# Performance work log

Hardware: AMD Instinct MI355X
Metric: run time of the kernel (lower is better)

## Reference

```python
import jax, jax.numpy as jnp
import numpy as np

N_NODES = 46080   # 512 graphs x 90 nodes
NPG = 90          # nodes per graph (AAL atlas)
G = 512           # number of graphs
E = 737280        # edges (degree 16)
IN_DIM = 90
H = 64            # hidden_channels
K = 70            # sort-pool k


def setup_inputs() -> dict:
    key = jax.random.key(0)
    ks = jax.random.split(key, 12)
    x = jax.random.normal(ks[0], (N_NODES, IN_DIM), dtype=jnp.float32)
    # intra-graph random edges: src/dst within each graph's 90-node block
    gidx = jnp.repeat(jnp.arange(G, dtype=jnp.int64), E // G) * NPG
    src = jax.random.randint(ks[1], (E,), 0, NPG, dtype=jnp.int64) + gidx
    dst = jax.random.randint(ks[2], (E,), 0, NPG, dtype=jnp.int64) + gidx
    edge_index = jnp.stack([src, dst])
    edge_weight = jax.random.uniform(ks[3], (E,), dtype=jnp.float32)
    batch = jnp.repeat(jnp.arange(G, dtype=jnp.int64), NPG)
    s1 = 1.0 / np.sqrt(IN_DIM)
    s2 = 1.0 / np.sqrt(H)
    sk = 1.0 / np.sqrt(H * K)
    W1 = jax.random.uniform(ks[4], (IN_DIM, H), jnp.float32, -s1, s1)
    b1 = jnp.zeros((H,), jnp.float32)
    W2 = jax.random.uniform(ks[5], (H, H), jnp.float32, -s2, s2)
    b2 = jnp.zeros((H,), jnp.float32)
    lw1 = jax.random.uniform(ks[6], (H * K, H), jnp.float32, -sk, sk)
    lb1 = jax.random.uniform(ks[7], (H,), jnp.float32, -sk, sk)
    lw2 = jax.random.uniform(ks[8], (H, 1), jnp.float32, -s2, s2)
    lb2 = jax.random.uniform(ks[9], (1,), jnp.float32, -s2, s2)
    return {"x": x, "edge_index": edge_index, "edge_weight": edge_weight,
            "batch": batch, "W1": W1, "b1": b1, "W2": W2, "b2": b2,
            "lw1": lw1, "lb1": lb1, "lw2": lw2, "lb2": lb2}


def _gcn_conv(x, W, b, src, dst, ew, n):
    # PyG GCNConv: add self-loops (weight 1), symmetric normalization,
    # message = norm * (x @ W)[src], scatter-add to dst, add bias.
    xw = x @ W
    loop = jnp.arange(n)
    src_f = jnp.concatenate([src, loop])
    dst_f = jnp.concatenate([dst, loop])
    ew_f = jnp.concatenate([ew, jnp.ones((n,), x.dtype)])
    deg = jax.ops.segment_sum(ew_f, dst_f, num_segments=n)
    dinv = jnp.where(deg > 0, jax.lax.rsqrt(jnp.maximum(deg, 1e-12)), 0.0)
    norm = dinv[src_f] * ew_f * dinv[dst_f]
    msg = xw[src_f] * norm[:, None]          # [E+n, H] irregular gather
    out = jax.ops.segment_sum(msg, dst_f, num_segments=n)
    return out + b


def reference(x, edge_index, edge_weight, batch, W1, b1, W2, b2, lw1, lb1, lw2, lb2):
    src, dst = edge_index[0], edge_index[1]
    h1 = _gcn_conv(x, W1, b1, src, dst, edge_weight, N_NODES)
    x_train = h1
    h = jax.nn.relu(h1)
    h2 = _gcn_conv(h, W2, b2, src, dst, edge_weight, N_NODES)
    # global_sort_pool: per graph, sort nodes descending by last channel, keep top K.
    # batch is contiguous with NPG nodes/graph, so a reshape is exact.
    hg = h2.reshape(G, NPG, H)
    order = jnp.argsort(-hg[:, :, -1], axis=1)          # [G, NPG] descending
    hs = jnp.take_along_axis(hg, order[:, :, None], axis=1)
    pooled = hs[:, :K, :].reshape(G, K * H)
    # F.dropout(p=0.5, training=False) -> identity at inference
    z = pooled @ lw1 + lb1
    z = z @ lw2 + lb2
    out = jax.nn.sigmoid(z).squeeze(-1)                  # [G]
    return out, x_train
```

## Files before the change

### kernel.cpp

```cpp
#include <hip/hip_runtime.h>


#define NG      512
#define NPG     90
#define EPG     1440
#define IN_DIM  90
#define HD      64
#define KP      70
#define E_TOT   (NG*EPG)
#define NT      512

__global__ __launch_bounds__(256) void weff_fold(
    const float* __restrict__ lw1, const float* __restrict__ lb1,
    const float* __restrict__ lw2, const float* __restrict__ lb2,
    float* __restrict__ ws)
{
    int i = blockIdx.x*256 + threadIdx.x;
    if (i < KP*HD) {
        const float4* row = (const float4*)(lw1 + (size_t)i*HD);
        const float4* w   = (const float4*)lw2;
        float s = 0.f;
        #pragma unroll
        for (int j4 = 0; j4 < HD/4; ++j4) {
            float4 r = row[j4], v = w[j4];
            s += r.x*v.x + r.y*v.y + r.z*v.z + r.w*v.w;
        }
        ws[i] = s;
    } else if (i == KP*HD) {
        float s = lb2[0];
        for (int j = 0; j < HD; ++j) s += lb1[j]*lw2[j];
        ws[KP*HD] = s;
    }
}

__global__ __launch_bounds__(NT, 4) void dgcnn_fused(
    const float* __restrict__ x,
    const int*   __restrict__ ei,
    const float* __restrict__ ew,
    const float* __restrict__ W1,
    const float* __restrict__ b1,
    const float* __restrict__ W2,
    const float* __restrict__ b2,
    const float* __restrict__ weff,
    float* __restrict__ out,
    float* __restrict__ xtrain)
{
    __shared__ float sB[NPG*HD];
    __shared__ float sC[NPG*HD];
    __shared__ float s_dinv[NPG];
    __shared__ int   s_indeg[NPG];
    __shared__ int   s_cursor[NPG];
    __shared__ int   s_rowstart[NPG+1];
    __shared__ unsigned s_epack[EPG];
    __shared__ int   s_ranknode[KP];
    __shared__ float s_red[8];

    const int g = blockIdx.x;
    const int t = threadIdx.x;
    const int j = t & 63;
    const int grp = t >> 6;
    const int ebase = g*EPG;
    const int nbase = g*NPG;

    if (t < NPG) { s_dinv[t] = 1.0f; s_indeg[t] = 0; }
    __syncthreads();

    for (int e = t; e < EPG; e += NT) {
        int d = ei[E_TOT + ebase + e] - nbase;
        float w = ew[ebase + e];
        atomicAdd(&s_dinv[d], w);
        atomicAdd(&s_indeg[d], 1);
    }
    for (int i4 = t; i4 < IN_DIM*HD/4; i4 += NT)
        ((float4*)sC)[i4] = ((const float4*)W1)[i4];
    __syncthreads();

    if (t < NPG) s_dinv[t] = rsqrtf(fmaxf(s_dinv[t], 1e-12f));
    if (t <= NPG) {
        int acc = 0;
        for (int i = 0; i < t; ++i) acc += s_indeg[i];
        s_rowstart[t] = acc;
        if (t < NPG) s_cursor[t] = acc;
    }
    __syncthreads();

    for (int e = t; e < EPG; e += NT) {
        int s = ei[ebase + e] - nbase;
        int d = ei[E_TOT + ebase + e] - nbase;
        float nrm = s_dinv[s] * ew[ebase + e] * s_dinv[d];
        int pos = atomicAdd(&s_cursor[d], 1);
        s_epack[pos] = (__float_as_uint(nrm) & ~127u) | (unsigned)s;
    }
    __syncthreads();

    const float* xg = x + (size_t)nbase * IN_DIM;
    for (int it = 0; it < 3; ++it) {
        int r0 = it*32 + grp*4;
        int rr0 = min(r0+0, NPG-1), rr1 = min(r0+1, NPG-1);
        int rr2 = min(r0+2, NPG-1), rr3 = min(r0+3, NPG-1);
        const float2* xp0 = (const float2*)(xg + rr0*IN_DIM);
        const float2* xp1 = (const float2*)(xg + rr1*IN_DIM);
        const float2* xp2 = (const float2*)(xg + rr2*IN_DIM);
        const float2* xp3 = (const float2*)(xg + rr3*IN_DIM);
        float a0 = 0.f, a1 = 0.f, a2 = 0.f, a3 = 0.f;
        #pragma unroll 9
        for (int kh = 0; kh < IN_DIM/2; ++kh) {
            float w0 = sC[(2*kh)*HD + j];
            float w1 = sC[(2*kh+1)*HD + j];
            float2 v0 = xp0[kh], v1 = xp1[kh], v2 = xp2[kh], v3 = xp3[kh];
            a0 += v0.x*w0 + v0.y*w1;
            a1 += v1.x*w0 + v1.y*w1;
            a2 += v2.x*w0 + v2.y*w1;
            a3 += v3.x*w0 + v3.y*w1;
        }
        if (r0+0 < NPG) sB[(r0+0)*HD + j] = a0;
        if (r0+1 < NPG) sB[(r0+1)*HD + j] = a1;
        if (r0+2 < NPG) sB[(r0+2)*HD + j] = a2;
        if (r0+3 < NPG) sB[(r0+3)*HD + j] = a3;
    }
    __syncthreads();

    float* xt = xtrain + (size_t)nbase * HD;
    for (int o = t; o < NPG*HD; o += NT) {
        int d = o >> 6, c = o & 63;
        float dv = s_dinv[d];
        float a = dv*dv*sB[o];
        int p0 = s_rowstart[d], p1 = s_rowstart[d+1];
        for (int p = p0; p < p1; ++p) {
            unsigned u = s_epack[p];
            a += __uint_as_float(u & ~127u) * sB[(int)(u & 127u)*HD + c];
        }
        a += b1[c];
        xt[o] = a;
        sC[o] = fmaxf(a, 0.f);
    }
    __syncthreads();

    for (int it = 0; it < 3; ++it) {
        int r0 = it*32 + grp*4;
        int rr0 = min(r0+0, NPG-1), rr1 = min(r0+1, NPG-1);
        int rr2 = min(r0+2, NPG-1), rr3 = min(r0+3, NPG-1);
        float a0 = 0.f, a1 = 0.f, a2 = 0.f, a3 = 0.f;
        #pragma unroll 4
        for (int k4 = 0; k4 < HD/4; ++k4) {
            int k = k4*4;
            float4 h0 = *(const float4*)&sC[rr0*HD + k];
            float4 h1 = *(const float4*)&sC[rr1*HD + k];
            float4 h2 = *(const float4*)&sC[rr2*HD + k];
            float4 h3 = *(const float4*)&sC[rr3*HD + k];
            float w0 = W2[(k+0)*HD + j];
            float w1 = W2[(k+1)*HD + j];
            float w2 = W2[(k+2)*HD + j];
            float w3 = W2[(k+3)*HD + j];
            a0 += h0.x*w0 + h0.y*w1 + h0.z*w2 + h0.w*w3;
            a1 += h1.x*w0 + h1.y*w1 + h1.z*w2 + h1.w*w3;
            a2 += h2.x*w0 + h2.y*w1 + h2.z*w2 + h2.w*w3;
            a3 += h3.x*w0 + h3.y*w1 + h3.z*w2 + h3.w*w3;
        }
        if (r0+0 < NPG) sB[(r0+0)*HD + j] = a0;
        if (r0+1 < NPG) sB[(r0+1)*HD + j] = a1;
        if (r0+2 < NPG) sB[(r0+2)*HD + j] = a2;
        if (r0+3 < NPG) sB[(r0+3)*HD + j] = a3;
    }
    __syncthreads();

    for (int o = t; o < NPG*HD; o += NT) {
        int d = o >> 6, c = o & 63;
        float dv = s_dinv[d];
        float a = dv*dv*sB[o];
        int p0 = s_rowstart[d], p1 = s_rowstart[d+1];
        for (int p = p0; p < p1; ++p) {
            unsigned u = s_epack[p];
            a += __uint_as_float(u & ~127u) * sB[(int)(u & 127u)*HD + c];
        }
        sC[o] = a + b2[c];
    }
    __syncthreads();

    if (t < NPG) {
        float vi = sC[t*HD + (HD-1)];
        int rank = 0;
        for (int jj = 0; jj < NPG; ++jj) {
            float vj = sC[jj*HD + (HD-1)];
            rank += (vj > vi) || (vj == vi && jj < t);
        }
        if (rank < KP) s_ranknode[rank] = t;
    }
    __syncthreads();

    float part = 0.f;
    #pragma unroll
    for (int m = 0; m < 9; ++m) {
        int i = t + m*NT;
        if (i < KP*HD) {
            int k = i >> 6, c = i & 63;
            part += weff[i] * sC[s_ranknode[k]*HD + c];
        }
    }
    #pragma unroll
    for (int off = 32; off > 0; off >>= 1) part += __shfl_down(part, off, 64);
    if (j == 0) s_red[grp] = part;
    __syncthreads();
    if (t == 0) {
        float zz = weff[KP*HD];
        #pragma unroll
        for (int m = 0; m < 8; ++m) zz += s_red[m];
        out[g] = 1.0f / (1.0f + expf(-zz));
    }
}

extern "C" void kernel_launch(void* const* d_in, const int* in_sizes, int n_in,
                              void* d_out, int out_size, void* d_ws, size_t ws_size,
                              hipStream_t stream) {
    const float* x   = (const float*)d_in[0];
    const int*   ei  = (const int*)  d_in[1];
    const float* ew  = (const float*)d_in[2];
    const float* W1  = (const float*)d_in[4];
    const float* b1  = (const float*)d_in[5];
    const float* W2  = (const float*)d_in[6];
    const float* b2  = (const float*)d_in[7];
    const float* lw1 = (const float*)d_in[8];
    const float* lb1 = (const float*)d_in[9];
    const float* lw2 = (const float*)d_in[10];
    const float* lb2 = (const float*)d_in[11];

    float* ws     = (float*)d_ws;
    float* out    = (float*)d_out;
    float* xtrain = out + NG;

    weff_fold<<<(KP*HD + 256)/256, 256, 0, stream>>>(lw1, lb1, lw2, lb2, ws);
    dgcnn_fused<<<NG, NT, 0, stream>>>(x, ei, ew, W1, b1, W2, b2,
                                       ws, out, xtrain);
}
```

Before: 182.3 us.

## Double block size to 1024 threads and parallelize scan, rank and W2 staging

Raises threads per block from 512 to 1024 so each graph's dense transforms, aggregation and readout use more lanes. The serial per-thread prefix sum over in-degrees becomes a wave-level shuffle scan, and the O(N^2) rank computation for sort-pooling is split across 8 lanes per node with a shuffle reduction. W2 is staged into shared memory instead of being read from global memory inside the inner loop. The larger block and extra shared memory lower how many blocks fit per CU and add register pressure under the 1024-thread launch bound, which may reduce occupancy.

After: 254.8 us. 1.4x slower.

```diff
diff --git a/kernel.cpp b/kernel.cpp
--- a/kernel.cpp
+++ b/kernel.cpp
@@ -8,7 +8,7 @@
 #define HD      64
 #define KP      70
 #define E_TOT   (NG*EPG)
-#define NT      512
+#define NT      1024
 
 __global__ __launch_bounds__(256) void weff_fold(
     const float* __restrict__ lw1, const float* __restrict__ lb1,
@@ -33,7 +33,7 @@
     }
 }
 
-__global__ __launch_bounds__(NT, 4) void dgcnn_fused(
+__global__ __launch_bounds__(NT, 8) void dgcnn_fused(
     const float* __restrict__ x,
     const int*   __restrict__ ei,
     const float* __restrict__ ew,
@@ -47,13 +47,15 @@
 {
     __shared__ float sB[NPG*HD];
     __shared__ float sC[NPG*HD];
+    __shared__ float sW2[HD*HD];
     __shared__ float s_dinv[NPG];
     __shared__ int   s_indeg[NPG];
     __shared__ int   s_cursor[NPG];
     __shared__ int   s_rowstart[NPG+1];
     __shared__ unsigned s_epack[EPG];
     __shared__ int   s_ranknode[KP];
-    __shared__ float s_red[8];
+    __shared__ float s_red[16];
+    __shared__ int   s_itmp;
 
     const int g = blockIdx.x;
     const int t = threadIdx.x;
@@ -76,11 +78,22 @@
     __syncthreads();
 
     if (t < NPG) s_dinv[t] = rsqrtf(fmaxf(s_dinv[t], 1e-12f));
-    if (t <= NPG) {
-        int acc = 0;
-        for (int i = 0; i < t; ++i) acc += s_indeg[i];
-        s_rowstart[t] = acc;
-        if (t < NPG) s_cursor[t] = acc;
+    {
+        int vi = (t < NPG) ? s_indeg[t] : 0;
+        int inc = vi;
+        #pragma unroll
+        for (int d = 1; d < 64; d <<= 1) {
+            int up = __shfl_up(inc, d, 64);
+            if ((t & 63) >= d) inc += up;
+        }
+        if (t == 63) s_itmp = inc;
+        __syncthreads();
+        if (t <= NPG) {
+            int base = (grp == 1) ? s_itmp : 0;
+            int excl = inc - vi + base;
+            s_rowstart[t] = excl;
+            if (t < NPG) s_cursor[t] = excl;
+        }
     }
     __syncthreads();
 
@@ -94,29 +107,31 @@
     __syncthreads();
 
     const float* xg = x + (size_t)nbase * IN_DIM;
-    for (int it = 0; it < 3; ++it) {
-        int r0 = it*32 + grp*4;
-        int rr0 = min(r0+0, NPG-1), rr1 = min(r0+1, NPG-1);
-        int rr2 = min(r0+2, NPG-1), rr3 = min(r0+3, NPG-1);
-        const float2* xp0 = (const float2*)(xg + rr0*IN_DIM);
-        const float2* xp1 = (const float2*)(xg + rr1*IN_DIM);
-        const float2* xp2 = (const float2*)(xg + rr2*IN_DIM);
-        const float2* xp3 = (const float2*)(xg + rr3*IN_DIM);
-        float a0 = 0.f, a1 = 0.f, a2 = 0.f, a3 = 0.f;
-        #pragma unroll 9
-        for (int kh = 0; kh < IN_DIM/2; ++kh) {
-            float w0 = sC[(2*kh)*HD + j];
-            float w1 = sC[(2*kh+1)*HD + j];
-            float2 v0 = xp0[kh], v1 = xp1[kh], v2 = xp2[kh], v3 = xp3[kh];
-            a0 += v0.x*w0 + v0.y*w1;
-            a1 += v1.x*w0 + v1.y*w1;
-            a2 += v2.x*w0 + v2.y*w1;
-            a3 += v3.x*w0 + v3.y*w1;
-        }
-        if (r0+0 < NPG) sB[(r0+0)*HD + j] = a0;
-        if (r0+1 < NPG) sB[(r0+1)*HD + j] = a1;
-        if (r0+2 < NPG) sB[(r0+2)*HD + j] = a2;
-        if (r0+3 < NPG) sB[(r0+3)*HD + j] = a3;
+    for (int it = 0; it < 2; ++it) {
+        int r0 = it*64 + grp*4;
+        if (r0 < NPG) {
+            int rr0 = min(r0+0, NPG-1), rr1 = min(r0+1, NPG-1);
+            int rr2 = min(r0+2, NPG-1), rr3 = min(r0+3, NPG-1);
+            const float2* xp0 = (const float2*)(xg + rr0*IN_DIM);
+            const float2* xp1 = (const float2*)(xg + rr1*IN_DIM);
+            const float2* xp2 = (const float2*)(xg + rr2*IN_DIM);
+            const float2* xp3 = (const float2*)(xg + rr3*IN_DIM);
+            float a0 = 0.f, a1 = 0.f, a2 = 0.f, a3 = 0.f;
+            #pragma unroll 9
+            for (int kh = 0; kh < IN_DIM/2; ++kh) {
+                float w0 = sC[(2*kh)*HD + j];
+                float w1 = sC[(2*kh+1)*HD + j];
+                float2 v0 = xp0[kh], v1 = xp1[kh], v2 = xp2[kh], v3 = xp3[kh];
+                a0 += v0.x*w0 + v0.y*w1;
+                a1 += v1.x*w0 + v1.y*w1;
+                a2 += v2.x*w0 + v2.y*w1;
+                a3 += v3.x*w0 + v3.y*w1;
+            }
+            if (r0+0 < NPG) sB[(r0+0)*HD + j] = a0;
+            if (r0+1 < NPG) sB[(r0+1)*HD + j] = a1;
+            if (r0+2 < NPG) sB[(r0+2)*HD + j] = a2;
+            if (r0+3 < NPG) sB[(r0+3)*HD + j] = a3;
+        }
     }
     __syncthreads();
 
@@ -134,33 +149,37 @@
         xt[o] = a;
         sC[o] = fmaxf(a, 0.f);
     }
-    __syncthreads();
-
-    for (int it = 0; it < 3; ++it) {
-        int r0 = it*32 + grp*4;
-        int rr0 = min(r0+0, NPG-1), rr1 = min(r0+1, NPG-1);
-        int rr2 = min(r0+2, NPG-1), rr3 = min(r0+3, NPG-1);
-        float a0 = 0.f, a1 = 0.f, a2 = 0.f, a3 = 0.f;
-        #pragma unroll 4
-        for (int k4 = 0; k4 < HD/4; ++k4) {
-            int k = k4*4;
-            float4 h0 = *(const float4*)&sC[rr0*HD + k];
-            float4 h1 = *(const float4*)&sC[rr1*HD + k];
-            float4 h2 = *(const float4*)&sC[rr2*HD + k];
-            float4 h3 = *(const float4*)&sC[rr3*HD + k];
-            float w0 = W2[(k+0)*HD + j];
-            float w1 = W2[(k+1)*HD + j];
-            float w2 = W2[(k+2)*HD + j];
-            float w3 = W2[(k+3)*HD + j];
-            a0 += h0.x*w0 + h0.y*w1 + h0.z*w2 + h0.w*w3;
-            a1 += h1.x*w0 + h1.y*w1 + h1.z*w2 + h1.w*w3;
-            a2 += h2.x*w0 + h2.y*w1 + h2.z*w2 + h2.w*w3;
-            a3 += h3.x*w0 + h3.y*w1 + h3.z*w2 + h3.w*w3;
-        }
-        if (r0+0 < NPG) sB[(r0+0)*HD + j] = a0;
-        if (r0+1 < NPG) sB[(r0+1)*HD + j] = a1;
-        if (r0+2 < NPG) sB[(r0+2)*HD + j] = a2;
-        if (r0+3 < NPG) sB[(r0+3)*HD + j] = a3;
+    for (int i4 = t; i4 < HD*HD/4; i4 += NT)
+        ((float4*)sW2)[i4] = ((const float4*)W2)[i4];
+    __syncthreads();
+
+    for (int it = 0; it < 2; ++it) {
+        int r0 = it*64 + grp*4;
+        if (r0 < NPG) {
+            int rr0 = min(r0+0, NPG-1), rr1 = min(r0+1, NPG-1);
+            int rr2 = min(r0+2, NPG-1), rr3 = min(r0+3, NPG-1);
+            float a0 = 0.f, a1 = 0.f, a2 = 0.f, a3 = 0.f;
+            #pragma unroll 4
+            for (int k4 = 0; k4 < HD/4; ++k4) {
+                int k = k4*4;
+                float4 h0 = *(const float4*)&sC[rr0*HD + k];
+                float4 h1 = *(const float4*)&sC[rr1*HD + k];
+                float4 h2 = *(const float4*)&sC[rr2*HD + k];
+                float4 h3 = *(const float4*)&sC[rr3*HD + k];
+                float w0 = sW2[(k+0)*HD + j];
+                float w1 = sW2[(k+1)*HD + j];
+                float w2 = sW2[(k+2)*HD + j];
+                float w3 = sW2[(k+3)*HD + j];
+                a0 += h0.x*w0 + h0.y*w1 + h0.z*w2 + h0.w*w3;
+                a1 += h1.x*w0 + h1.y*w1 + h1.z*w2 + h1.w*w3;
+                a2 += h2.x*w0 + h2.y*w1 + h2.z*w2 + h2.w*w3;
+                a3 += h3.x*w0 + h3.y*w1 + h3.z*w2 + h3.w*w3;
+            }
+            if (r0+0 < NPG) sB[(r0+0)*HD + j] = a0;
+            if (r0+1 < NPG) sB[(r0+1)*HD + j] = a1;
+            if (r0+2 < NPG) sB[(r0+2)*HD + j] = a2;
+            if (r0+3 < NPG) sB[(r0+3)*HD + j] = a3;
+        }
     }
     __syncthreads();
 
@@ -177,20 +196,28 @@
     }
     __syncthreads();
 
-    if (t < NPG) {
-        float vi = sC[t*HD + (HD-1)];
-        int rank = 0;
-        for (int jj = 0; jj < NPG; ++jj) {
-            float vj = sC[jj*HD + (HD-1)];
-            rank += (vj > vi) || (vj == vi && jj < t);
-        }
-        if (rank < KP) s_ranknode[rank] = t;
+    if (t < NPG*8) {
+        int n = t >> 3, q = t & 7;
+        float vi = sC[n*HD + (HD-1)];
+        int cnt = 0;
+        #pragma unroll 12
+        for (int m = 0; m < 12; ++m) {
+            int jj = q*12 + m;
+            if (jj < NPG) {
+                float vj = sC[jj*HD + (HD-1)];
+                cnt += (vj > vi) || (vj == vi && jj < n);
+            }
+        }
+        cnt += __shfl_down(cnt, 4, 8);
+        cnt += __shfl_down(cnt, 2, 8);
+        cnt += __shfl_down(cnt, 1, 8);
+        if (q == 0 && cnt < KP) s_ranknode[cnt] = n;
     }
     __syncthreads();
 
     float part = 0.f;
     #pragma unroll
-    for (int m = 0; m < 9; ++m) {
+    for (int m = 0; m < 5; ++m) {
         int i = t + m*NT;
         if (i < KP*HD) {
             int k = i >> 6, c = i & 63;
@@ -204,7 +231,7 @@
     if (t == 0) {
         float zz = weff[KP*HD];
         #pragma unroll
-        for (int m = 0; m < 8; ++m) zz += s_red[m];
+        for (int m = 0; m < 16; ++m) zz += s_red[m];
         out[g] = 1.0f / (1.0f + expf(-zz));
     }
 }
```

## Split fused DGCNN kernel into CSR, GEMM, scatter and final-pool stages

Applied to the files above, without the earlier changes.

Breaks the single per-graph fused kernel into five launches: CSR and normalisation build (with the weight fold merged in), a row-tiled x@W1 GEMM, a first aggregation split four ways by column quarter, a row-tiled GEMM with ReLU, and a per-graph second aggregation with sort-pool and readout. The goal is far more, and lighter, blocks for the GEMMs and the first scatter than the 512 heavy-LDS blocks of the fused version. In exchange, intermediates (packed edges, row starts, xw, h@W2) make round trips through global memory and there are extra kernel launches.

Measured after the change: 177.5 us. 2.7% less time.

```diff
diff --git a/kernel.cpp b/kernel.cpp
--- a/kernel.cpp
+++ b/kernel.cpp
@@ -8,74 +8,36 @@
 #define HD      64
 #define KP      70
 #define E_TOT   (NG*EPG)
-#define NT      512
-
-__global__ __launch_bounds__(256) void weff_fold(
+
+#define WEFF_OFF   0
+#define EPACK_OFF  4608
+#define RS_OFF     (EPACK_OFF + NG*EPG)
+#define D2_OFF     (RS_OFF + NG*96)
+#define HW2_OFF    (D2_OFF + NG*96)
+
+__global__ __launch_bounds__(256) void k0_csr(
+    const int* __restrict__ ei, const float* __restrict__ ew,
     const float* __restrict__ lw1, const float* __restrict__ lb1,
     const float* __restrict__ lw2, const float* __restrict__ lb2,
     float* __restrict__ ws)
 {
-    int i = blockIdx.x*256 + threadIdx.x;
-    if (i < KP*HD) {
-        const float4* row = (const float4*)(lw1 + (size_t)i*HD);
-        const float4* w   = (const float4*)lw2;
-        float s = 0.f;
-        #pragma unroll
-        for (int j4 = 0; j4 < HD/4; ++j4) {
-            float4 r = row[j4], v = w[j4];
-            s += r.x*v.x + r.y*v.y + r.z*v.z + r.w*v.w;
-        }
-        ws[i] = s;
-    } else if (i == KP*HD) {
-        float s = lb2[0];
-        for (int j = 0; j < HD; ++j) s += lb1[j]*lw2[j];
-        ws[KP*HD] = s;
-    }
-}
-
-__global__ __launch_bounds__(NT, 4) void dgcnn_fused(
-    const float* __restrict__ x,
-    const int*   __restrict__ ei,
-    const float* __restrict__ ew,
-    const float* __restrict__ W1,
-    const float* __restrict__ b1,
-    const float* __restrict__ W2,
-    const float* __restrict__ b2,
-    const float* __restrict__ weff,
-    float* __restrict__ out,
-    float* __restrict__ xtrain)
-{
-    __shared__ float sB[NPG*HD];
-    __shared__ float sC[NPG*HD];
-    __shared__ float s_dinv[NPG];
+    __shared__ float s_deg[NPG];
     __shared__ int   s_indeg[NPG];
+    __shared__ int   s_rowstart[NPG+1];
     __shared__ int   s_cursor[NPG];
-    __shared__ int   s_rowstart[NPG+1];
-    __shared__ unsigned s_epack[EPG];
-    __shared__ int   s_ranknode[KP];
-    __shared__ float s_red[8];
-
-    const int g = blockIdx.x;
-    const int t = threadIdx.x;
-    const int j = t & 63;
-    const int grp = t >> 6;
-    const int ebase = g*EPG;
-    const int nbase = g*NPG;
-
-    if (t < NPG) { s_dinv[t] = 1.0f; s_indeg[t] = 0; }
-    __syncthreads();
-
-    for (int e = t; e < EPG; e += NT) {
+
+    const int g = blockIdx.x, t = threadIdx.x;
+    const int ebase = g*EPG, nbase = g*NPG;
+
+    if (t < NPG) { s_deg[t] = 1.0f; s_indeg[t] = 0; }
+    __syncthreads();
+    for (int e = t; e < EPG; e += 256) {
         int d = ei[E_TOT + ebase + e] - nbase;
-        float w = ew[ebase + e];
-        atomicAdd(&s_dinv[d], w);
+        atomicAdd(&s_deg[d], ew[ebase + e]);
         atomicAdd(&s_indeg[d], 1);
     }
-    for (int i4 = t; i4 < IN_DIM*HD/4; i4 += NT)
-        ((float4*)sC)[i4] = ((const float4*)W1)[i4];
-    __syncthreads();
-
-    if (t < NPG) s_dinv[t] = rsqrtf(fmaxf(s_dinv[t], 1e-12f));
+    __syncthreads();
+    if (t < NPG) s_deg[t] = rsqrtf(fmaxf(s_deg[t], 1e-12f));
     if (t <= NPG) {
         int acc = 0;
         for (int i = 0; i < t; ++i) acc += s_indeg[i];
@@ -84,93 +46,175 @@
     }
     __syncthreads();
 
-    for (int e = t; e < EPG; e += NT) {
+    unsigned* epk = (unsigned*)ws + EPACK_OFF + g*EPG;
+    for (int e = t; e < EPG; e += 256) {
         int s = ei[ebase + e] - nbase;
         int d = ei[E_TOT + ebase + e] - nbase;
-        float nrm = s_dinv[s] * ew[ebase + e] * s_dinv[d];
+        float nrm = s_deg[s] * ew[ebase + e] * s_deg[d];
         int pos = atomicAdd(&s_cursor[d], 1);
-        s_epack[pos] = (__float_as_uint(nrm) & ~127u) | (unsigned)s;
-    }
-    __syncthreads();
-
-    const float* xg = x + (size_t)nbase * IN_DIM;
-    for (int it = 0; it < 3; ++it) {
-        int r0 = it*32 + grp*4;
-        int rr0 = min(r0+0, NPG-1), rr1 = min(r0+1, NPG-1);
-        int rr2 = min(r0+2, NPG-1), rr3 = min(r0+3, NPG-1);
-        const float2* xp0 = (const float2*)(xg + rr0*IN_DIM);
-        const float2* xp1 = (const float2*)(xg + rr1*IN_DIM);
-        const float2* xp2 = (const float2*)(xg + rr2*IN_DIM);
-        const float2* xp3 = (const float2*)(xg + rr3*IN_DIM);
-        float a0 = 0.f, a1 = 0.f, a2 = 0.f, a3 = 0.f;
-        #pragma unroll 9
-        for (int kh = 0; kh < IN_DIM/2; ++kh) {
-            float w0 = sC[(2*kh)*HD + j];
-            float w1 = sC[(2*kh+1)*HD + j];
-            float2 v0 = xp0[kh], v1 = xp1[kh], v2 = xp2[kh], v3 = xp3[kh];
-            a0 += v0.x*w0 + v0.y*w1;
-            a1 += v1.x*w0 + v1.y*w1;
-            a2 += v2.x*w0 + v2.y*w1;
-            a3 += v3.x*w0 + v3.y*w1;
-        }
-        if (r0+0 < NPG) sB[(r0+0)*HD + j] = a0;
-        if (r0+1 < NPG) sB[(r0+1)*HD + j] = a1;
-        if (r0+2 < NPG) sB[(r0+2)*HD + j] = a2;
-        if (r0+3 < NPG) sB[(r0+3)*HD + j] = a3;
-    }
-    __syncthreads();
-
-    float* xt = xtrain + (size_t)nbase * HD;
-    for (int o = t; o < NPG*HD; o += NT) {
+        epk[pos] = (__float_as_uint(nrm) & ~127u) | (unsigned)s;
+    }
+    if (t <= NPG) ((int*)ws)[RS_OFF + g*96 + t] = s_rowstart[t];
+    if (t < NPG)  ws[D2_OFF + g*96 + t] = s_deg[t]*s_deg[t];
+
+    int i = g*256 + t;
+    if (g < 18) {
+        if (i < KP*HD) {
+            const float4* row = (const float4*)(lw1 + (size_t)i*HD);
+            const float4* w   = (const float4*)lw2;
+            float s = 0.f;
+            #pragma unroll
+            for (int j4 = 0; j4 < HD/4; ++j4) {
+                float4 r = row[j4], v = w[j4];
+                s += r.x*v.x + r.y*v.y + r.z*v.z + r.w*v.w;
+            }
+            ws[WEFF_OFF + i] = s;
+        } else if (i == KP*HD) {
+            float s = lb2[0];
+            for (int jj = 0; jj < HD; ++jj) s += lb1[jj]*lw2[jj];
+            ws[WEFF_OFF + KP*HD] = s;
+        }
+    }
+}
+
+__global__ __launch_bounds__(256) void k1_gemm1(
+    const float* __restrict__ x, const float* __restrict__ W1,
+    float* __restrict__ xw)
+{
+    __shared__ float sx[16*IN_DIM];
+    const int t = threadIdx.x;
+    const int row0 = blockIdx.x * 16;
+
+    const float4* gx = (const float4*)(x + (size_t)row0*IN_DIM);
+    for (int i = t; i < 16*IN_DIM/4; i += 256) ((float4*)sx)[i] = gx[i];
+    __syncthreads();
+
+    const int j = t & 63, rg = t >> 6;
+    float a0 = 0.f, a1 = 0.f, a2 = 0.f, a3 = 0.f;
+    const float2* xp0 = (const float2*)&sx[(rg*4+0)*IN_DIM];
+    const float2* xp1 = (const float2*)&sx[(rg*4+1)*IN_DIM];
+    const float2* xp2 = (const float2*)&sx[(rg*4+2)*IN_DIM];
+    const float2* xp3 = (const float2*)&sx[(rg*4+3)*IN_DIM];
+    #pragma unroll 9
+    for (int kh = 0; kh < IN_DIM/2; ++kh) {
+        float w0 = W1[(2*kh)*HD + j];
+        float w1 = W1[(2*kh+1)*HD + j];
+        float2 v0 = xp0[kh], v1 = xp1[kh], v2 = xp2[kh], v3 = xp3[kh];
+        a0 += v0.x*w0 + v0.y*w1;
+        a1 += v1.x*w0 + v1.y*w1;
+        a2 += v2.x*w0 + v2.y*w1;
+        a3 += v3.x*w0 + v3.y*w1;
+    }
+    float* o = xw + (size_t)(row0 + rg*4)*HD + j;
+    o[0*HD] = a0; o[1*HD] = a1; o[2*HD] = a2; o[3*HD] = a3;
+}
+
+__global__ __launch_bounds__(256) void k2_scatter1(
+    float* __restrict__ xt,
+    const float* __restrict__ b1,
+    const float* __restrict__ ws)
+{
+    __shared__ float    sxw[NPG*16];
+    __shared__ unsigned sep[EPG];
+    __shared__ int      srs[NPG+1];
+    __shared__ float    sd2[NPG];
+
+    const int t = threadIdx.x;
+    const int g = blockIdx.x >> 2, q = blockIdx.x & 3;
+    const int c0 = q*16, nbase = g*NPG;
+
+    const unsigned* epk = (const unsigned*)ws + EPACK_OFF + g*EPG;
+    for (int i = t; i < EPG; i += 256) sep[i] = epk[i];
+    if (t <= NPG) srs[t] = ((const int*)ws)[RS_OFF + g*96 + t];
+    if (t < NPG)  sd2[t] = ws[D2_OFF + g*96 + t];
+    for (int i = t; i < NPG*4; i += 256) {
+        int row = i >> 2, f = i & 3;
+        ((float4*)sxw)[i] = *(const float4*)(xt + (size_t)(nbase+row)*HD + c0 + f*4);
+    }
+    __syncthreads();
+
+    for (int o = t; o < NPG*16; o += 256) {
+        int d = o >> 4, c = o & 15;
+        float a = sd2[d]*sxw[o];
+        int p0 = srs[d], p1 = srs[d+1];
+        for (int p = p0; p < p1; ++p) {
+            unsigned u = sep[p];
+            a += __uint_as_float(u & ~127u) * sxw[(int)(u & 127u)*16 + c];
+        }
+        xt[(size_t)(nbase+d)*HD + c0 + c] = a + b1[c0+c];
+    }
+}
+
+__global__ __launch_bounds__(256) void k3_gemm2(
+    const float* __restrict__ xt, const float* __restrict__ W2,
+    float* __restrict__ ws)
+{
+    __shared__ float sh[16*HD];
+    const int t = threadIdx.x;
+    const int row0 = blockIdx.x * 16;
+
+    const float4* gh = (const float4*)(xt + (size_t)row0*HD);
+    for (int i = t; i < 16*HD/4; i += 256) {
+        float4 v = gh[i];
+        v.x = fmaxf(v.x, 0.f); v.y = fmaxf(v.y, 0.f);
+        v.z = fmaxf(v.z, 0.f); v.w = fmaxf(v.w, 0.f);
+        ((float4*)sh)[i] = v;
+    }
+    __syncthreads();
+
+    const int j = t & 63, rg = t >> 6;
+    float a0 = 0.f, a1 = 0.f, a2 = 0.f, a3 = 0.f;
+    #pragma unroll 4
+    for (int k4 = 0; k4 < HD/4; ++k4) {
+        int k = k4*4;
+        float4 h0 = *(const float4*)&sh[(rg*4+0)*HD + k];
+        float4 h1 = *(const float4*)&sh[(rg*4+1)*HD + k];
+        float4 h2 = *(const float4*)&sh[(rg*4+2)*HD + k];
+        float4 h3 = *(const float4*)&sh[(rg*4+3)*HD + k];
+        float w0 = W2[(k+0)*HD + j];
+        float w1 = W2[(k+1)*HD + j];
+        float w2 = W2[(k+2)*HD + j];
+        float w3 = W2[(k+3)*HD + j];
+        a0 += h0.x*w0 + h0.y*w1 + h0.z*w2 + h0.w*w3;
+        a1 += h1.x*w0 + h1.y*w1 + h1.z*w2 + h1.w*w3;
+        a2 += h2.x*w0 + h2.y*w1 + h2.z*w2 + h2.w*w3;
+        a3 += h3.x*w0 + h3.y*w1 + h3.z*w2 + h3.w*w3;
+    }
+    float* o = ws + HW2_OFF + (size_t)(row0 + rg*4)*HD + j;
+    o[0*HD] = a0; o[1*HD] = a1; o[2*HD] = a2; o[3*HD] = a3;
+}
+
+__global__ __launch_bounds__(512) void k4_final(
+    const float* __restrict__ b2,
+    const float* __restrict__ ws,
+    float* __restrict__ out)
+{
+    __shared__ float    sB[NPG*HD];
+    __shared__ float    sC[NPG*HD];
+    __shared__ unsigned sep[EPG];
+    __shared__ int      srs[NPG+1];
+    __shared__ float    sd2[NPG];
+    __shared__ int      s_ranknode[KP];
+    __shared__ float    s_red[8];
+
+    const int g = blockIdx.x, t = threadIdx.x;
+    const int j = t & 63, grp = t >> 6;
+    const int nbase = g*NPG;
+
+    const float4* gb = (const float4*)(ws + HW2_OFF + (size_t)nbase*HD);
+    for (int i = t; i < NPG*HD/4; i += 512) ((float4*)sB)[i] = gb[i];
+    const unsigned* epk = (const unsigned*)ws + EPACK_OFF + g*EPG;
+    for (int i = t; i < EPG; i += 512) sep[i] = epk[i];
+    if (t <= NPG) srs[t] = ((const int*)ws)[RS_OFF + g*96 + t];
+    if (t < NPG)  sd2[t] = ws[D2_OFF + g*96 + t];
+    __syncthreads();
+
+    for (int o = t; o < NPG*HD; o += 512) {
         int d = o >> 6, c = o & 63;
-        float dv = s_dinv[d];
-        float a = dv*dv*sB[o];
-        int p0 = s_rowstart[d], p1 = s_rowstart[d+1];
+        float a = sd2[d]*sB[o];
+        int p0 = srs[d], p1 = srs[d+1];
         for (int p = p0; p < p1; ++p) {
-            unsigned u = s_epack[p];
-            a += __uint_as_float(u & ~127u) * sB[(int)(u & 127u)*HD + c];
-        }
-        a += b1[c];
-        xt[o] = a;
-        sC[o] = fmaxf(a, 0.f);
-    }
-    __syncthreads();
-
-    for (int it = 0; it < 3; ++it) {
-        int r0 = it*32 + grp*4;
-        int rr0 = min(r0+0, NPG-1), rr1 = min(r0+1, NPG-1);
-        int rr2 = min(r0+2, NPG-1), rr3 = min(r0+3, NPG-1);
-        float a0 = 0.f, a1 = 0.f, a2 = 0.f, a3 = 0.f;
-        #pragma unroll 4
-        for (int k4 = 0; k4 < HD/4; ++k4) {
-            int k = k4*4;
-            float4 h0 = *(const float4*)&sC[rr0*HD + k];
-            float4 h1 = *(const float4*)&sC[rr1*HD + k];
-            float4 h2 = *(const float4*)&sC[rr2*HD + k];
-            float4 h3 = *(const float4*)&sC[rr3*HD + k];
-            float w0 = W2[(k+0)*HD + j];
-            float w1 = W2[(k+1)*HD + j];
-            float w2 = W2[(k+2)*HD + j];
-            float w3 = W2[(k+3)*HD + j];
-            a0 += h0.x*w0 + h0.y*w1 + h0.z*w2 + h0.w*w3;
-            a1 += h1.x*w0 + h1.y*w1 + h1.z*w2 + h1.w*w3;
-            a2 += h2.x*w0 + h2.y*w1 + h2.z*w2 + h2.w*w3;
-            a3 += h3.x*w0 + h3.y*w1 + h3.z*w2 + h3.w*w3;
-        }
-        if (r0+0 < NPG) sB[(r0+0)*HD + j] = a0;
-        if (r0+1 < NPG) sB[(r0+1)*HD + j] = a1;
-        if (r0+2 < NPG) sB[(r0+2)*HD + j] = a2;
-        if (r0+3 < NPG) sB[(r0+3)*HD + j] = a3;
-    }
-    __syncthreads();
-
-    for (int o = t; o < NPG*HD; o += NT) {
-        int d = o >> 6, c = o & 63;
-        float dv = s_dinv[d];
-        float a = dv*dv*sB[o];
-        int p0 = s_rowstart[d], p1 = s_rowstart[d+1];
-        for (int p = p0; p < p1; ++p) {
-            unsigned u = s_epack[p];
+            unsigned u = sep[p];
             a += __uint_as_float(u & ~127u) * sB[(int)(u & 127u)*HD + c];
         }
         sC[o] = a + b2[c];
@@ -191,10 +235,10 @@
     float part = 0.f;
     #pragma unroll
     for (int m = 0; m < 9; ++m) {
-        int i = t + m*NT;
+        int i = t + m*512;
         if (i < KP*HD) {
             int k = i >> 6, c = i & 63;
-            part += weff[i] * sC[s_ranknode[k]*HD + c];
+            part += ws[WEFF_OFF + i] * sC[s_ranknode[k]*HD + c];
         }
     }
     #pragma unroll
@@ -202,7 +246,7 @@
     if (j == 0) s_red[grp] = part;
     __syncthreads();
     if (t == 0) {
-        float zz = weff[KP*HD];
+        float zz = ws[WEFF_OFF + KP*HD];
         #pragma unroll
         for (int m = 0; m < 8; ++m) zz += s_red[m];
         out[g] = 1.0f / (1.0f + expf(-zz));
@@ -228,7 +272,9 @@
     float* out    = (float*)d_out;
     float* xtrain = out + NG;
 
-    weff_fold<<<(KP*HD + 256)/256, 256, 0, stream>>>(lw1, lb1, lw2, lb2, ws);
-    dgcnn_fused<<<NG, NT, 0, stream>>>(x, ei, ew, W1, b1, W2, b2,
-                                       ws, out, xtrain);
-}
+    k0_csr    <<<NG,   256, 0, stream>>>(ei, ew, lw1, lb1, lw2, lb2, ws);
+    k1_gemm1  <<<2880, 256, 0, stream>>>(x, W1, xtrain);
+    k2_scatter1<<<NG*4, 256, 0, stream>>>(xtrain, b1, ws);
+    k3_gemm2  <<<2880, 256, 0, stream>>>(xtrain, W2, ws);
+    k4_final  <<<NG,   512, 0, stream>>>(b2, ws, out);
+}
```
